# Performance work log

Hardware: AMD Instinct MI355X
Metric: run time of the kernel (lower is better)

## Reference

```python
import jax, jax.numpy as jnp
import numpy as np

B, C, F = 8192, 2048, 2048


def setup_inputs() -> dict:
    key = jax.random.key(0)
    k1, k2 = jax.random.split(key)
    x = jax.random.normal(k1, (B, F), dtype=jnp.float32)
    means = jax.random.normal(k2, (C, F), dtype=jnp.float32)
    # scalar 'variance' parameter used as a divisor (std); realistic post-update value
    variance = jnp.ones((1,), dtype=jnp.float32)
    return {"x": x, "means": means, "variance": variance}


def reference(x, means, variance):
    # non-deep_nno, eval-mode branch: x = x / std with std = variance param
    xs = x / variance  # [B, F]
    # L2 distance to class means via GEMM cdist: ||a-b|| = sqrt(||a||^2 + ||b||^2 - 2 a.b)
    x2 = jnp.sum(xs * xs, axis=1, keepdims=True)          # [B, 1]
    m2 = jnp.sum(means * means, axis=1)                    # [C]
    cross = jnp.einsum('bf,cf->bc', xs, means)             # [B, C] GEMM
    d2 = jnp.maximum(x2 + m2[None, :] - 2.0 * cross, 0.0)  # clamp fp error
    cumulative_diff = jnp.sqrt(d2)                         # torch.norm(diff, p=2, dim=2)
    exponent = -cumulative_diff
    probs = jax.nn.softmax(exponent, axis=1)
    return (probs, exponent, cumulative_diff)
```

## Files before the change

kernel.cpp:

```cpp
#include <hip/hip_runtime.h>
#include <hip/hip_bf16.h>

constexpr int BB = 8192;
constexpr int CC = 2048;
constexpr int FF = 2048;

typedef __bf16 bf16x8 __attribute__((ext_vector_type(8)));
typedef float  f32x4  __attribute__((ext_vector_type(4)));

typedef __attribute__((address_space(1))) unsigned int gu32;
typedef __attribute__((address_space(3))) unsigned int lu32;

__device__ __forceinline__ void async_copy16(const void* g, void* l) {
    __builtin_amdgcn_global_load_lds(
        (gu32*)(unsigned long long)g,
        (lu32*)(unsigned int)(unsigned long long)l,
        16, 0, 0);
}

__global__ void prep_rows(const float* __restrict__ x,
                          const float* __restrict__ means,
                          unsigned short* __restrict__ xb,
                          unsigned short* __restrict__ mb,
                          float* __restrict__ x2,
                          float* __restrict__ m2,
                          const float* __restrict__ varp) {
    const int blk = blockIdx.x;
    const bool isx = blk < BB;
    const int row = isx ? blk : blk - BB;
    const int t = threadIdx.x;
    const float scale = isx ? (1.0f / varp[0]) : 1.0f;
    const float* in = isx ? x : means;
    unsigned short* outb = isx ? xb : mb;
    const size_t base = (size_t)row * FF + (size_t)t * 8;
    const float4 a = *(const float4*)(in + base);
    const float4 b = *(const float4*)(in + base + 4);
    float v[8] = {a.x * scale, a.y * scale, a.z * scale, a.w * scale,
                  b.x * scale, b.y * scale, b.z * scale, b.w * scale};
    float s = 0.0f;
    bf16x8 h;
#pragma unroll
    for (int i = 0; i < 8; ++i) {
        s += v[i] * v[i];
        h[i] = (__bf16)v[i];
    }
    *(bf16x8*)(outb + base) = h;
#pragma unroll
    for (int off = 32; off > 0; off >>= 1) s += __shfl_down(s, off);
    __shared__ float red[4];
    if ((t & 63) == 0) red[t >> 6] = s;
    __syncthreads();
    if (t == 0) {
        float tot = (red[0] + red[1]) + (red[2] + red[3]);
        if (isx) x2[row] = tot; else m2[row] = tot;
    }
}

__global__ __launch_bounds__(256, 2) void gemm_epi(
    const unsigned short* __restrict__ A,
    const unsigned short* __restrict__ Bm,
    const float* __restrict__ x2,
    const float* __restrict__ m2,
    float* __restrict__ expo,
    float* __restrict__ cum) {
    __shared__ __align__(16) unsigned short As[128 * 32];
    __shared__ __align__(16) unsigned short Bs[128 * 32];

    const int t = threadIdx.x;
    const int wave = t >> 6, lane = t & 63;
    const int bx = blockIdx.x;
    const int bm = ((bx >> 7) << 3) | (bx & 7);
    const int bn = (bx >> 3) & 15;
    const int wm = wave >> 1, wn = wave & 1;
    const int rowA0 = bm * 128, rowB0 = bn * 128;

    const int srow = lane >> 2;
    const int scol = (((lane & 3) ^ ((lane >> 3) & 3))) * 8;

    const int rl = lane & 15;
    const int kphys = (((lane >> 4) ^ ((rl >> 1) & 3))) * 8;
    const int ar = wm * 64 + rl;
    const int br = wn * 64 + rl;

    f32x4 acc[4][4] = {};

    for (int k0 = 0; k0 < FF; k0 += 32) {
#pragma unroll
        for (int r = 0; r < 2; ++r) {
            const int chunk = r * 4 + wave;
            const int rr = chunk * 16 + srow;
            async_copy16(&A[(size_t)(rowA0 + rr) * FF + k0 + scol], &As[chunk * 512]);
            async_copy16(&Bm[(size_t)(rowB0 + rr) * FF + k0 + scol], &Bs[chunk * 512]);
        }
        __syncthreads();

        bf16x8 af[4], bf[4];
#pragma unroll
        for (int i = 0; i < 4; ++i) af[i] = *(const bf16x8*)&As[(ar + i * 16) * 32 + kphys];
#pragma unroll
        for (int j = 0; j < 4; ++j) bf[j] = *(const bf16x8*)&Bs[(br + j * 16) * 32 + kphys];
#pragma unroll
        for (int i = 0; i < 4; ++i)
#pragma unroll
            for (int j = 0; j < 4; ++j)
                acc[i][j] = __builtin_amdgcn_mfma_f32_16x16x32_bf16(af[i], bf[j], acc[i][j], 0, 0, 0);
        __syncthreads();
    }

    const int ln = lane & 15, lq = lane >> 4;
    const int grow0 = rowA0 + wm * 64 + lq * 4;
    const int gcol0 = rowB0 + wn * 64 + ln;
    float x2v[16];
#pragma unroll
    for (int i = 0; i < 4; ++i)
#pragma unroll
        for (int r = 0; r < 4; ++r) x2v[i * 4 + r] = x2[grow0 + i * 16 + r];
    float m2v[4];
#pragma unroll
    for (int j = 0; j < 4; ++j) m2v[j] = m2[gcol0 + j * 16];

#pragma unroll
    for (int i = 0; i < 4; ++i)
#pragma unroll
        for (int j = 0; j < 4; ++j)
#pragma unroll
            for (int r = 0; r < 4; ++r) {
                const float d2 = x2v[i * 4 + r] + m2v[j] - 2.0f * acc[i][j][r];
                const float d = sqrtf(fmaxf(d2, 0.0f));
                const size_t idx = (size_t)(grow0 + i * 16 + r) * CC + (gcol0 + j * 16);
                __builtin_nontemporal_store(d, &cum[idx]);
                expo[idx] = -d;
            }
}

__global__ void softmax_rows(const float* __restrict__ e, float* __restrict__ p) {
    const int row = blockIdx.x;
    const int t = threadIdx.x;
    const size_t base = (size_t)row * CC + (size_t)t * 8;
    const float4 a = *(const float4*)(e + base);
    const float4 b = *(const float4*)(e + base + 4);
    float v[8] = {a.x, a.y, a.z, a.w, b.x, b.y, b.z, b.w};

    float mx = v[0];
#pragma unroll
    for (int i = 1; i < 8; ++i) mx = fmaxf(mx, v[i]);
#pragma unroll
    for (int off = 32; off > 0; off >>= 1) mx = fmaxf(mx, __shfl_down(mx, off));
    __shared__ float redm[4], reds[4];
    if ((t & 63) == 0) redm[t >> 6] = mx;
    __syncthreads();
    mx = fmaxf(fmaxf(redm[0], redm[1]), fmaxf(redm[2], redm[3]));

    float ev[8];
    float s = 0.0f;
#pragma unroll
    for (int i = 0; i < 8; ++i) {
        ev[i] = __expf(v[i] - mx);
        s += ev[i];
    }
#pragma unroll
    for (int off = 32; off > 0; off >>= 1) s += __shfl_down(s, off);
    if ((t & 63) == 0) reds[t >> 6] = s;
    __syncthreads();
    s = (reds[0] + reds[1]) + (reds[2] + reds[3]);
    const float inv = 1.0f / s;

    float4 o0 = {ev[0] * inv, ev[1] * inv, ev[2] * inv, ev[3] * inv};
    float4 o1 = {ev[4] * inv, ev[5] * inv, ev[6] * inv, ev[7] * inv};
    *(float4*)(p + base) = o0;
    *(float4*)(p + base + 4) = o1;
}

extern "C" void kernel_launch(void* const* d_in, const int* in_sizes, int n_in,
                              void* d_out, int out_size, void* d_ws, size_t ws_size,
                              hipStream_t stream) {
    const float* x     = (const float*)d_in[0];
    const float* means = (const float*)d_in[1];
    const float* var   = (const float*)d_in[2];
    float* out = (float*)d_out;

    unsigned short* xb = (unsigned short*)d_ws;
    unsigned short* mb = xb + (size_t)BB * FF;
    float* x2 = (float*)(mb + (size_t)CC * FF);
    float* m2 = x2 + BB;

    float* probs = out;
    float* expo  = out + (size_t)BB * CC;
    float* cum   = expo + (size_t)BB * CC;

    prep_rows<<<BB + CC, 256, 0, stream>>>(x, means, xb, mb, x2, m2, var);
    gemm_epi<<<(BB / 128) * (CC / 128), 256, 0, stream>>>(xb, mb, x2, m2, expo, cum);
    softmax_rows<<<BB, 256, 0, stream>>>(expo, probs);
}
```

Before: 349.7 us.

## Double GEMM K-tile to 64, drop softmax max pass, nontemporal prob stores

```diff
diff --git a/kernel.cpp b/kernel.cpp
--- a/kernel.cpp
+++ b/kernel.cpp
@@ -63,8 +63,8 @@
     const float* __restrict__ m2,
     float* __restrict__ expo,
     float* __restrict__ cum) {
-    __shared__ __align__(16) unsigned short As[128 * 32];
-    __shared__ __align__(16) unsigned short Bs[128 * 32];
+    __shared__ __align__(16) unsigned short As[128 * 64];
+    __shared__ __align__(16) unsigned short Bs[128 * 64];
 
     const int t = threadIdx.x;
     const int wave = t >> 6, lane = t & 63;
@@ -74,36 +74,40 @@
     const int wm = wave >> 1, wn = wave & 1;
     const int rowA0 = bm * 128, rowB0 = bn * 128;
 
-    const int srow = lane >> 2;
-    const int scol = (((lane & 3) ^ ((lane >> 3) & 3))) * 8;
+    const int sr = lane >> 3;
+    const int sc = ((lane & 7) ^ sr) * 8;
 
     const int rl = lane & 15;
-    const int kphys = (((lane >> 4) ^ ((rl >> 1) & 3))) * 8;
+    const int kb = lane >> 4;
     const int ar = wm * 64 + rl;
     const int br = wn * 64 + rl;
 
     f32x4 acc[4][4] = {};
 
-    for (int k0 = 0; k0 < FF; k0 += 32) {
+    for (int k0 = 0; k0 < FF; k0 += 64) {
 #pragma unroll
-        for (int r = 0; r < 2; ++r) {
+        for (int r = 0; r < 4; ++r) {
             const int chunk = r * 4 + wave;
-            const int rr = chunk * 16 + srow;
-            async_copy16(&A[(size_t)(rowA0 + rr) * FF + k0 + scol], &As[chunk * 512]);
-            async_copy16(&Bm[(size_t)(rowB0 + rr) * FF + k0 + scol], &Bs[chunk * 512]);
+            const int rr = chunk * 8 + sr;
+            async_copy16(&A[(size_t)(rowA0 + rr) * FF + k0 + sc], &As[chunk * 512]);
+            async_copy16(&Bm[(size_t)(rowB0 + rr) * FF + k0 + sc], &Bs[chunk * 512]);
         }
         __syncthreads();
 
-        bf16x8 af[4], bf[4];
 #pragma unroll
-        for (int i = 0; i < 4; ++i) af[i] = *(const bf16x8*)&As[(ar + i * 16) * 32 + kphys];
+        for (int s = 0; s < 2; ++s) {
+            const int pc = ((s * 4 + kb) ^ (lane & 7)) * 8;
+            bf16x8 af[4], bf[4];
 #pragma unroll
-        for (int j = 0; j < 4; ++j) bf[j] = *(const bf16x8*)&Bs[(br + j * 16) * 32 + kphys];
+            for (int i = 0; i < 4; ++i) af[i] = *(const bf16x8*)&As[(ar + i * 16) * 64 + pc];
 #pragma unroll
-        for (int i = 0; i < 4; ++i)
+            for (int j = 0; j < 4; ++j) bf[j] = *(const bf16x8*)&Bs[(br + j * 16) * 64 + pc];
 #pragma unroll
-            for (int j = 0; j < 4; ++j)
-                acc[i][j] = __builtin_amdgcn_mfma_f32_16x16x32_bf16(af[i], bf[j], acc[i][j], 0, 0, 0);
+            for (int i = 0; i < 4; ++i)
+#pragma unroll
+                for (int j = 0; j < 4; ++j)
+                    acc[i][j] = __builtin_amdgcn_mfma_f32_16x16x32_bf16(af[i], bf[j], acc[i][j], 0, 0, 0);
+        }
         __syncthreads();
     }
 
@@ -139,36 +143,23 @@
     const size_t base = (size_t)row * CC + (size_t)t * 8;
     const float4 a = *(const float4*)(e + base);
     const float4 b = *(const float4*)(e + base + 4);
-    float v[8] = {a.x, a.y, a.z, a.w, b.x, b.y, b.z, b.w};
-
-    float mx = v[0];
-#pragma unroll
-    for (int i = 1; i < 8; ++i) mx = fmaxf(mx, v[i]);
-#pragma unroll
-    for (int off = 32; off > 0; off >>= 1) mx = fmaxf(mx, __shfl_down(mx, off));
-    __shared__ float redm[4], reds[4];
-    if ((t & 63) == 0) redm[t >> 6] = mx;
-    __syncthreads();
-    mx = fmaxf(fmaxf(redm[0], redm[1]), fmaxf(redm[2], redm[3]));
-
-    float ev[8];
+    float ev[8] = {__expf(a.x), __expf(a.y), __expf(a.z), __expf(a.w),
+                   __expf(b.x), __expf(b.y), __expf(b.z), __expf(b.w)};
     float s = 0.0f;
 #pragma unroll
-    for (int i = 0; i < 8; ++i) {
-        ev[i] = __expf(v[i] - mx);
-        s += ev[i];
-    }
+    for (int i = 0; i < 8; ++i) s += ev[i];
 #pragma unroll
     for (int off = 32; off > 0; off >>= 1) s += __shfl_down(s, off);
+    __shared__ float reds[4];
     if ((t & 63) == 0) reds[t >> 6] = s;
     __syncthreads();
     s = (reds[0] + reds[1]) + (reds[2] + reds[3]);
     const float inv = 1.0f / s;
 
-    float4 o0 = {ev[0] * inv, ev[1] * inv, ev[2] * inv, ev[3] * inv};
-    float4 o1 = {ev[4] * inv, ev[5] * inv, ev[6] * inv, ev[7] * inv};
-    *(float4*)(p + base) = o0;
-    *(float4*)(p + base + 4) = o1;
+    f32x4 o0 = {ev[0] * inv, ev[1] * inv, ev[2] * inv, ev[3] * inv};
+    f32x4 o1 = {ev[4] * inv, ev[5] * inv, ev[6] * inv, ev[7] * inv};
+    __builtin_nontemporal_store(o0, (f32x4*)(p + base));
+    __builtin_nontemporal_store(o1, (f32x4*)(p + base + 4));
 }
 
 extern "C" void kernel_launch(void* const* d_in, const int* in_sizes, int n_in,
```

New measurement: 336.6 us. -3.7%, faster.
